# Performance work log

Measured on AMD Instinct MI355X. Metric: run time of the kernel, lower is better.

Reference implementation:

```python
import jax, jax.numpy as jnp
import numpy as np

DIM = 3072
HEADS = 24
HEAD_DIM = 128
MLP_HIDDEN = int(DIM * 3.0)   # 9216
EPS = 1e-6
B, S = 1, 4096


def setup_inputs() -> dict:
    key = jax.random.key(0)
    ks = jax.random.split(key, 9)
    fused_out = 3 * DIM + 2 * MLP_HIDDEN  # 27648
    std_in = 1.0 / np.sqrt(DIM)
    return {
        "hidden_states": jax.random.normal(ks[0], (B, S, DIM), jnp.float32),
        "temb_mod": jax.random.normal(ks[1], (B, 3 * DIM), jnp.float32),
        "rotary_cos": jax.random.uniform(ks[2], (S, HEAD_DIM), jnp.float32),
        "rotary_sin": jax.random.uniform(ks[3], (S, HEAD_DIM), jnp.float32),
        "w_qkv_mlp": jax.random.normal(ks[4], (DIM, fused_out), jnp.float32) * std_in,
        "w_out_attn": jax.random.normal(ks[5], (DIM, DIM), jnp.float32) * std_in,
        "w_out_mlp": jax.random.normal(ks[6], (MLP_HIDDEN, DIM), jnp.float32) * (1.0 / np.sqrt(MLP_HIDDEN)),
        "norm_q_w": jnp.ones((HEAD_DIM,), jnp.float32),
        "norm_k_w": jnp.ones((HEAD_DIM,), jnp.float32),
    }


def _rms_norm(x, w):
    var = jnp.mean(jnp.square(x), axis=-1, keepdims=True)
    return x * jax.lax.rsqrt(var + EPS) * w


def _apply_rope(x, cos, sin):
    # x: [B,H,S,D]; cos/sin: [S,D]. Interleaved (diffusers FLUX) rotation.
    xr = x.reshape(*x.shape[:-1], HEAD_DIM // 2, 2)
    x_re, x_im = xr[..., 0], xr[..., 1]
    x_rot = jnp.stack([-x_im, x_re], axis=-1).reshape(x.shape)
    return x * cos + x_rot * sin


def reference(hidden_states, temb_mod, rotary_cos, rotary_sin,
              w_qkv_mlp, w_out_attn, w_out_mlp, norm_q_w, norm_k_w):
    residual = hidden_states
    # modulation split: shift, scale, gate each [B,1,D]
    shift, scale, gate = jnp.split(temb_mod[:, None, :], 3, axis=-1)
    # LayerNorm (no affine)
    mu = jnp.mean(hidden_states, axis=-1, keepdims=True)
    var = jnp.mean(jnp.square(hidden_states - mu), axis=-1, keepdims=True)
    ln = (hidden_states - mu) * jax.lax.rsqrt(var + EPS)
    h = ln * (1.0 + scale) + shift
    # fused QKV + MLP projection
    qkv_mlp = jnp.einsum('bsd,df->bsf', h, w_qkv_mlp)
    qkv, mlp_gate_up = jnp.split(qkv_mlp, [3 * DIM], axis=-1)
    q, k, v = jnp.split(qkv, 3, axis=-1)
    to_heads = lambda t: t.reshape(B, S, HEADS, HEAD_DIM).transpose(0, 2, 1, 3)
    q, k, v = to_heads(q), to_heads(k), to_heads(v)
    q = _apply_rope(_rms_norm(q, norm_q_w), rotary_cos, rotary_sin)
    k = _apply_rope(_rms_norm(k, norm_k_w), rotary_cos, rotary_sin)
    # attention
    scores = jnp.einsum('bhqd,bhkd->bhqk', q, k) / np.sqrt(HEAD_DIM).astype(np.float32)
    attn = jnp.einsum('bhqk,bhkd->bhqd', jax.nn.softmax(scores, axis=-1), v)
    attn = attn.transpose(0, 2, 1, 3).reshape(B, S, DIM)
    # SwiGLU
    a, b = jnp.split(mlp_gate_up, 2, axis=-1)
    mlp_out = jax.nn.silu(a) * b
    out = jnp.einsum('bsd,de->bse', attn, w_out_attn) + jnp.einsum('bsm,md->bsd', mlp_out, w_out_mlp)
    return residual + gate * out
```

## Files before the change

kernel.cpp:

```cpp
#include <hip/hip_runtime.h>
#include <stdint.h>
#include <math.h>

#define DIM 3072
#define SEQ 4096
#define NH 24
#define HD 128
#define MLP 9216
#define FUSED 27648
#define SD FUSED
#define K2 12288

typedef __attribute__((ext_vector_type(8))) short short8;
typedef __attribute__((ext_vector_type(4))) float f32x4;

__device__ __forceinline__ float bf2f(uint16_t b){ uint32_t x = ((uint32_t)b)<<16; return __builtin_bit_cast(float,x); }
__device__ __forceinline__ uint16_t f2bf(float f){
  uint32_t x = __builtin_bit_cast(uint32_t,f);
  x += 0x7fffu + ((x>>16)&1u);
  return (uint16_t)(x>>16);
}
__device__ __forceinline__ void gl_lds16(const void* g, void* l){
  __builtin_amdgcn_global_load_lds((const __attribute__((address_space(1))) void*)g,
                                   (__attribute__((address_space(3))) void*)l, 16, 0, 0);
}

__global__ __launch_bounds__(256) void castT_kernel(const float* __restrict__ src,
                                                    uint16_t* __restrict__ dst,
                                                    int K, int N, int dstStride){
  __shared__ float tile[32][33];
  int t = threadIdx.x;
  int n0 = blockIdx.x<<5, k0 = blockIdx.y<<5;
  int r = t>>3, c4 = (t&7)<<2;
  float4 v = *(const float4*)&src[(size_t)(k0+r)*N + n0 + c4];
  tile[r][c4] = v.x; tile[r][c4+1] = v.y; tile[r][c4+2] = v.z; tile[r][c4+3] = v.w;
  __syncthreads();
  int n = t>>3, kc = (t&7)<<2;
  ushort4 o;
  o.x = f2bf(tile[kc  ][n]);
  o.y = f2bf(tile[kc+1][n]);
  o.z = f2bf(tile[kc+2][n]);
  o.w = f2bf(tile[kc+3][n]);
  *(ushort4*)&dst[(size_t)(n0+n)*dstStride + k0 + kc] = o;
}

__global__ __launch_bounds__(256) void ln_mod_kernel(const float* __restrict__ x,
                                                     const float* __restrict__ temb,
                                                     uint16_t* __restrict__ h){
  int s = blockIdx.x;
  int t = threadIdx.x;
  const float4* row = (const float4*)(x + (size_t)s*DIM);
  float4 v[3];
  float sum=0.f, ss=0.f;
  #pragma unroll
  for (int i=0;i<3;i++){
    v[i] = row[t + i*256];
    sum += v[i].x+v[i].y+v[i].z+v[i].w;
    ss  += v[i].x*v[i].x + v[i].y*v[i].y + v[i].z*v[i].z + v[i].w*v[i].w;
  }
  #pragma unroll
  for (int off=32; off; off>>=1){ sum += __shfl_xor(sum, off, 64); ss += __shfl_xor(ss, off, 64); }
  __shared__ float red[8];
  int lane = t&63, w = t>>6;
  if (lane==0){ red[w]=sum; red[w+4]=ss; }
  __syncthreads();
  sum = red[0]+red[1]+red[2]+red[3];
  ss  = red[4]+red[5]+red[6]+red[7];
  float mu = sum*(1.f/DIM);
  float var = ss*(1.f/DIM) - mu*mu;
  float rs = rsqrtf(var + 1e-6f);
  uint16_t* hrow = h + (size_t)s*DIM;
  #pragma unroll
  for (int i=0;i<3;i++){
    int c = (t + i*256)*4;
    float4 sc = *(const float4*)&temb[DIM + c];
    float4 sh = *(const float4*)&temb[c];
    ushort4 o;
    o.x = f2bf((v[i].x - mu)*rs*(1.f+sc.x) + sh.x);
    o.y = f2bf((v[i].y - mu)*rs*(1.f+sc.y) + sh.y);
    o.z = f2bf((v[i].z - mu)*rs*(1.f+sc.z) + sh.z);
    o.w = f2bf((v[i].w - mu)*rs*(1.f+sc.w) + sh.w);
    *(ushort4*)&hrow[c] = o;
  }
}

#define STAGE_HT(SRC, LDSB, KOFF) do{ \
    gl_lds16((SRC) + (KOFF), (LDSB) + (size_t)t*8); \
    gl_lds16((SRC) + r64K + (KOFF), (LDSB) + (size_t)(t+512)*8); \
  }while(0)

#define GPHASE(MI0, MI1, STG, WAITV) do{ \
    short8 a00 = *(const short8*)&Ab[(MI0)*1024 + pk0]; \
    short8 a01 = *(const short8*)&Ab[(MI0)*1024 + pk1]; \
    short8 a10 = *(const short8*)&Ab[(MI1)*1024 + pk0]; \
    short8 a11 = *(const short8*)&Ab[(MI1)*1024 + pk1]; \
    STG; \
    __builtin_amdgcn_s_barrier(); \
    asm volatile("s_waitcnt lgkmcnt(0)" ::: "memory"); \
    __builtin_amdgcn_s_setprio(1); \
    _Pragma("unroll") \
    for (int ni=0; ni<4; ni++){ \
      acc[MI0][ni] = __builtin_amdgcn_mfma_f32_16x16x32_bf16(a00, bfr[ni][0], acc[MI0][ni], 0,0,0); \
      acc[MI1][ni] = __builtin_amdgcn_mfma_f32_16x16x32_bf16(a10, bfr[ni][0], acc[MI1][ni], 0,0,0); \
      acc[MI0][ni] = __builtin_amdgcn_mfma_f32_16x16x32_bf16(a01, bfr[ni][1], acc[MI0][ni], 0,0,0); \
      acc[MI1][ni] = __builtin_amdgcn_mfma_f32_16x16x32_bf16(a11, bfr[ni][1], acc[MI1][ni], 0,0,0); \
    } \
    __builtin_amdgcn_s_setprio(0); \
    WAITV \
    __builtin_amdgcn_s_barrier(); \
  }while(0)

template<bool OUT_BF16, bool FINAL>
__global__ __launch_bounds__(512,2) void gemm256_kernel(const uint16_t* __restrict__ A,
                                                        const uint16_t* __restrict__ BT,
                                                        void* __restrict__ Cout,
                                                        const float* __restrict__ resid,
                                                        const float* __restrict__ temb,
                                                        int M, int N, int K){
  __shared__ alignas(16) uint16_t As[2][2][128*64];
  __shared__ alignas(16) uint16_t Bs[2][2][128*64];
  const int t = threadIdx.x, lane = t&63, w = t>>6;
  const int G = gridDim.x, cpx = G>>3;
  const int b = blockIdx.x;
  const int b2 = (b&7)*cpx + (b>>3);
  const int mt = M>>8;
  const int n_t = b2/mt, m_t = b2 - n_t*mt;
  const size_t m0 = (size_t)m_t<<8, n0 = (size_t)n_t<<8;
  const int wm = (w>>2)<<7, wn = (w&3)<<6;
  const int lr = lane&15, q4 = lane>>4;
  const int r0 = t>>3;
  const int g0 = (t&7) ^ (r0&7);
  const uint16_t* Asrc = A  + (m0 + r0)*(size_t)K + g0*8;
  const uint16_t* Bsrc = BT + (n0 + r0)*(size_t)K + g0*8;
  const size_t r64K = (size_t)64*K, r128K = (size_t)128*K;
  const int halfA = w>>2, halfB = (w&3)>>1, rbB = wn&64;
  const uint16_t* ArdBase = &As[0][halfA][0] + lr*64;
  const uint16_t* BrdBase = &Bs[0][halfB][0] + (rbB+lr)*64;
  const int x7 = lr&7;
  const int pk0 = (q4^x7)<<3, pk1 = ((q4|4)^x7)<<3;
  STAGE_HT(Bsrc, &Bs[0][0][0], (size_t)0);
  STAGE_HT(Bsrc, &Bs[0][1][0], r128K);
  STAGE_HT(Asrc, &As[0][0][0], (size_t)0);
  STAGE_HT(Asrc, &As[0][1][0], r128K);
  STAGE_HT(Bsrc, &Bs[1][0][0], (size_t)64);
  STAGE_HT(Bsrc, &Bs[1][1][0], r128K + 64);
  asm volatile("s_waitcnt vmcnt(4)" ::: "memory");
  __builtin_amdgcn_s_barrier();
  f32x4 acc[8][4] = {};
  const int NT = K>>6;
  for (int T=0; T<NT; ++T){
    const int cur = T&1, nxt = cur^1;
    const uint16_t* Ab = ArdBase + (cur<<14);
    const uint16_t* Bb = BrdBase + (cur<<14);
    uint16_t* AsN0 = &As[nxt][0][0]; uint16_t* AsN1 = &As[nxt][1][0];
    uint16_t* BsC0 = &Bs[cur][0][0]; uint16_t* BsC1 = &Bs[cur][1][0];
    const bool stA = (T+1<NT), stB = (T+2<NT);
    const size_t kA = (size_t)(T+1)<<6, kB = (size_t)(T+2)<<6;
    short8 bfr[4][2];
    #pragma unroll
    for (int ni=0; ni<4; ni++){
      bfr[ni][0] = *(const short8*)&Bb[ni*1024 + pk0];
      bfr[ni][1] = *(const short8*)&Bb[ni*1024 + pk1];
    }
    GPHASE(0,1, if(stA){ STAGE_HT(Asrc, AsN0, kA); }, ;);
    GPHASE(2,3, if(stA){ STAGE_HT(Asrc, AsN1, kA + r128K); }, ;);
    GPHASE(4,5, if(stB){ STAGE_HT(Bsrc, BsC0, kB); }, ;);
    GPHASE(6,7, if(stB){ STAGE_HT(Bsrc, BsC1, kB + r128K); },
           if(stB){ asm volatile("s_waitcnt vmcnt(4)" ::: "memory"); }
           else   { asm volatile("s_waitcnt vmcnt(0)" ::: "memory"); });
  }
  #pragma unroll
  for (int mi=0; mi<8; mi++){
    #pragma unroll
    for (int ni=0; ni<4; ni++){
      const size_t col = n0 + wn + ni*16 + lr;
      const float gate = FINAL ? temb[2*DIM + col] : 0.f;
      #pragma unroll
      for (int r=0; r<4; r++){
        const size_t row = m0 + wm + mi*16 + (q4<<2) + r;
        const size_t idx = row*(size_t)N + col;
        float vv = acc[mi][ni][r];
        if (FINAL) vv = resid[idx] + gate*vv;
        if (OUT_BF16) ((uint16_t*)Cout)[idx] = f2bf(vv);
        else          ((float*)Cout)[idx] = vv;
      }
    }
  }
}

__global__ __launch_bounds__(256) void qk_rope_kernel(uint16_t* __restrict__ qkv,
                                                      const float* __restrict__ cosb,
                                                      const float* __restrict__ sinb,
                                                      const float* __restrict__ wq,
                                                      const float* __restrict__ wk){
  int t = threadIdx.x, lane = t&63, w = t>>6;
  int pair = blockIdx.x*4 + w;
  int s = pair/24, hh = pair - s*24;
  int d0 = lane*2;
  float c0 = cosb[s*HD + d0], c1 = cosb[s*HD + d0+1];
  float sn0 = sinb[s*HD + d0], sn1 = sinb[s*HD + d0+1];
  #pragma unroll
  for (int which=0; which<2; ++which){
    uint16_t* p = qkv + (size_t)s*SD + which*DIM + hh*HD + d0;
    const float* ww = which ? wk : wq;
    uint32_t u = *(const uint32_t*)p;
    float x0 = bf2f((uint16_t)(u&0xffffu)), x1 = bf2f((uint16_t)(u>>16));
    float ssum = x0*x0 + x1*x1;
    #pragma unroll
    for (int off=32; off; off>>=1) ssum += __shfl_xor(ssum, off, 64);
    float r = rsqrtf(ssum*(1.f/HD) + 1e-6f);
    float xn0 = x0*r*ww[d0], xn1 = x1*r*ww[d0+1];
    float y0 = xn0*c0 - xn1*sn0;
    float y1 = xn1*c1 + xn0*sn1;
    *(uint32_t*)p = (uint32_t)f2bf(y0) | ((uint32_t)f2bf(y1)<<16);
  }
}

__global__ __launch_bounds__(256) void attn_kernel(const uint16_t* __restrict__ qkv,
                                                   uint16_t* __restrict__ out){
  __shared__ alignas(16) uint16_t QP[64*128];
  __shared__ alignas(16) uint16_t Ks[64*128];
  __shared__ alignas(16) uint16_t Vt[128*64];
  int t = threadIdx.x, lane = t&63, w = t>>6;
  int q0 = blockIdx.x<<6, h = blockIdx.y;
  int lr = lane&15, q4 = lane>>4, lk = q4<<3;
  const uint16_t* qb = qkv + (size_t)q0*SD + h*HD;
  #pragma unroll
  for (int i=0;i<4;i++){
    int c = t + i*256;
    gl_lds16((const char*)(qb + (size_t)(c>>4)*SD) + ((c&15)<<4), (char*)QP + c*16);
  }
  __syncthreads();
  short8 qf[4];
  #pragma unroll
  for (int kc=0;kc<4;kc++) qf[kc] = *(const short8*)&QP[(w*16+lr)*128 + kc*32 + lk];
  __syncthreads();
  float m_q = -3.0e38f, l_q = 0.f;
  f32x4 o[8] = {};
  const uint16_t* kb = qkv + (size_t)DIM + h*HD;
  const uint16_t* vb = qkv + (size_t)(2*DIM) + h*HD;
  uint16_t* Pw = QP + w*(16*64);
  const float scale = 0.08838834764831845f;
  for (int kt=0; kt<64; ++kt){
    const uint16_t* kbt = kb + (size_t)(kt<<6)*SD;
    const uint16_t* vbt = vb + (size_t)(kt<<6)*SD;
    __syncthreads();
    #pragma unroll
    for (int i=0;i<4;i++){
      int c = t + i*256;
      int row = c>>4, gd = c&15;
      gl_lds16((const char*)(kbt + (size_t)row*SD) + (((gd ^ (row&15))&15)<<4),
               (char*)Ks + c*16);
    }
    #pragma unroll
    for (int i=0;i<8;i++){
      int idx = t + i*256;
      int rp = idx>>6;
      int k0 = rp<<1, d0 = lane<<1;
      uint32_t u0 = *(const uint32_t*)(vbt + (size_t)k0*SD + d0);
      uint32_t u1 = *(const uint32_t*)(vbt + (size_t)(k0+1)*SD + d0);
      int pos = (((rp>>2) ^ (lane&7))<<3) + (k0&7);
      *(uint32_t*)&Vt[(d0<<6) + pos]     = (u0&0xffffu) | (u1<<16);
      *(uint32_t*)&Vt[((d0+1)<<6) + pos] = (u0>>16) | (u1&0xffff0000u);
    }
    __syncthreads();
    f32x4 ta[4];
    __builtin_amdgcn_s_setprio(1);
    #pragma unroll
    for (int nk=0;nk<4;nk++){
      ta[nk] = (f32x4){0.f,0.f,0.f,0.f};
      #pragma unroll
      for (int kc=0;kc<4;kc++){
        short8 kf = *(const short8*)&Ks[(nk*16+lr)*128 + (((kc*4+q4) ^ lr)<<3)];
        ta[nk] = __builtin_amdgcn_mfma_f32_16x16x32_bf16(kf, qf[kc], ta[nk], 0,0,0);
      }
      ta[nk] *= scale;
    }
    __builtin_amdgcn_s_setprio(0);
    float mx01 = fmaxf(fmaxf(ta[0][0],ta[0][1]), fmaxf(ta[0][2],ta[0][3]));
    float mx23 = fmaxf(fmaxf(ta[1][0],ta[1][1]), fmaxf(ta[1][2],ta[1][3]));
    float mx45 = fmaxf(fmaxf(ta[2][0],ta[2][1]), fmaxf(ta[2][2],ta[2][3]));
    float mx67 = fmaxf(fmaxf(ta[3][0],ta[3][1]), fmaxf(ta[3][2],ta[3][3]));
    float pmax = fmaxf(fmaxf(mx01,mx23), fmaxf(mx45,mx67));
    pmax = fmaxf(pmax, __shfl_xor(pmax, 16, 64));
    pmax = fmaxf(pmax, __shfl_xor(pmax, 32, 64));
    int skip = __all(pmax <= m_q + 8.f);
    float alpha_q = 1.f;
    if (!skip){
      float mnew = fmaxf(m_q, pmax);
      alpha_q = __expf(m_q - mnew);
      m_q = mnew;
    }
    float psum = 0.f;
    #pragma unroll
    for (int nk=0;nk<4;nk++){
      float p0 = __expf(ta[nk][0] - m_q);
      float p1 = __expf(ta[nk][1] - m_q);
      float p2 = __expf(ta[nk][2] - m_q);
      float p3 = __expf(ta[nk][3] - m_q);
      psum += (p0+p1)+(p2+p3);
      uint32_t lo = (uint32_t)f2bf(p0) | ((uint32_t)f2bf(p1)<<16);
      uint32_t hi = (uint32_t)f2bf(p2) | ((uint32_t)f2bf(p3)<<16);
      int k0 = nk*16 + (q4<<2);
      uint2 pk; pk.x = lo; pk.y = hi;
      *(uint2*)&Pw[lr*64 + ((((k0>>3) ^ lr)&7)<<3) + (k0&7)] = pk;
    }
    psum += __shfl_xor(psum, 16, 64);
    psum += __shfl_xor(psum, 32, 64);
    l_q = l_q*alpha_q + psum;
    if (!skip){
      float aR0 = __shfl(alpha_q, (q4<<2)+0, 64);
      float aR1 = __shfl(alpha_q, (q4<<2)+1, 64);
      float aR2 = __shfl(alpha_q, (q4<<2)+2, 64);
      float aR3 = __shfl(alpha_q, (q4<<2)+3, 64);
      #pragma unroll
      for (int nd=0;nd<8;nd++){
        f32x4 t4 = o[nd];
        t4[0]*=aR0; t4[1]*=aR1; t4[2]*=aR2; t4[3]*=aR3;
        o[nd]=t4;
      }
    }
    __builtin_amdgcn_s_setprio(1);
    #pragma unroll
    for (int kc=0;kc<2;kc++){
      short8 pf = *(const short8*)&Pw[lr*64 + ((((kc*4+q4) ^ lr)&7)<<3)];
      #pragma unroll
      for (int nd=0;nd<8;nd++){
        int d = nd*16 + lr;
        short8 vf = *(const short8*)&Vt[(d<<6) + ((((kc*4+q4) ^ ((lr>>1)&7)))<<3)];
        o[nd] = __builtin_amdgcn_mfma_f32_16x16x32_bf16(pf, vf, o[nd], 0,0,0);
      }
    }
    __builtin_amdgcn_s_setprio(0);
  }
  float linv0 = 1.f/__shfl(l_q, (q4<<2)+0, 64);
  float linv1 = 1.f/__shfl(l_q, (q4<<2)+1, 64);
  float linv2 = 1.f/__shfl(l_q, (q4<<2)+2, 64);
  float linv3 = 1.f/__shfl(l_q, (q4<<2)+3, 64);
  uint16_t* ob = out + (size_t)(q0 + w*16)*K2 + h*HD;
  #pragma unroll
  for (int nd=0;nd<8;nd++){
    ob[(size_t)(q4*4 + 0)*K2 + nd*16 + lr] = f2bf(o[nd][0]*linv0);
    ob[(size_t)(q4*4 + 1)*K2 + nd*16 + lr] = f2bf(o[nd][1]*linv1);
    ob[(size_t)(q4*4 + 2)*K2 + nd*16 + lr] = f2bf(o[nd][2]*linv2);
    ob[(size_t)(q4*4 + 3)*K2 + nd*16 + lr] = f2bf(o[nd][3]*linv3);
  }
}

__global__ __launch_bounds__(256) void swiglu_kernel(const uint16_t* __restrict__ qkv,
                                                     uint16_t* __restrict__ mlp){
  size_t idx = ((size_t)blockIdx.x*256 + threadIdx.x)*4;
  size_t s = idx/MLP, j = idx - s*MLP;
  const uint16_t* pa = qkv + s*SD + 3*DIM + j;
  const uint16_t* pb = pa + MLP;
  ushort4 ua = *(const ushort4*)pa, ub = *(const ushort4*)pb;
  ushort4 o;
  float a, b;
  a = bf2f(ua.x); b = bf2f(ub.x); o.x = f2bf(a*b/(1.f+__expf(-a)));
  a = bf2f(ua.y); b = bf2f(ub.y); o.y = f2bf(a*b/(1.f+__expf(-a)));
  a = bf2f(ua.z); b = bf2f(ub.z); o.z = f2bf(a*b/(1.f+__expf(-a)));
  a = bf2f(ua.w); b = bf2f(ub.w); o.w = f2bf(a*b/(1.f+__expf(-a)));
  *(ushort4*)(mlp + s*K2 + j) = o;
}

extern "C" void kernel_launch(void* const* d_in, const int* in_sizes, int n_in,
                              void* d_out, int out_size, void* d_ws, size_t ws_size,
                              hipStream_t stream){
  (void)in_sizes; (void)n_in; (void)out_size;
  const float* hs   = (const float*)d_in[0];
  const float* temb = (const float*)d_in[1];
  const float* rcos = (const float*)d_in[2];
  const float* rsin = (const float*)d_in[3];
  const float* w1   = (const float*)d_in[4];
  const float* wa   = (const float*)d_in[5];
  const float* wm   = (const float*)d_in[6];
  const float* nqw  = (const float*)d_in[7];
  const float* nkw  = (const float*)d_in[8];

  char* ws = (char*)d_ws;
  const size_t off_w1T  = 0;
  const size_t off_woT  = 169869312ULL;
  const size_t off_h    = 245366784ULL;
  const size_t off_qkv  = 270532608ULL;
  const size_t off_ap   = 497025024ULL;
  const size_t needed   = 597688320ULL;
  if (ws_size < needed) return;

  uint16_t* w1T  = (uint16_t*)(ws + off_w1T);
  uint16_t* woT  = (uint16_t*)(ws + off_woT);
  uint16_t* hbuf = (uint16_t*)(ws + off_h);
  uint16_t* qkv  = (uint16_t*)(ws + off_qkv);
  uint16_t* ap   = (uint16_t*)(ws + off_ap);

  castT_kernel<<<dim3(FUSED/32, DIM/32), 256, 0, stream>>>(w1, w1T, DIM, FUSED, DIM);
  castT_kernel<<<dim3(DIM/32,  DIM/32),  256, 0, stream>>>(wa, woT, DIM, DIM, K2);
  castT_kernel<<<dim3(DIM/32,  MLP/32),  256, 0, stream>>>(wm, woT + DIM, MLP, DIM, K2);
  ln_mod_kernel<<<SEQ, 256, 0, stream>>>(hs, temb, hbuf);
  gemm256_kernel<true,false><<<(SEQ/256)*(FUSED/256), 512, 0, stream>>>(hbuf, w1T, qkv, nullptr, nullptr, SEQ, FUSED, DIM);
  qk_rope_kernel<<<SEQ*NH/4, 256, 0, stream>>>(qkv, rcos, rsin, nqw, nkw);
  attn_kernel<<<dim3(SEQ/64, NH), 256, 0, stream>>>(qkv, ap);
  swiglu_kernel<<<(SEQ*(size_t)MLP/4)/256, 256, 0, stream>>>(qkv, ap + DIM);
  gemm256_kernel<false,true><<<(SEQ/256)*(DIM/256), 512, 0, stream>>>(ap, woT, d_out, hs, temb, SEQ, DIM, K2);
}
```

Measured before the change: 2.289 ms.

## Double-buffer K/V tiles in attention to overlap loads with MFMA compute

The attention kernel now keeps two LDS buffers each for K and transposed V. It issues the next tile's K global-to-LDS loads and V register loads before computing on the current tile, then writes the transposed V into the alternate buffer after the PV MFMAs. This hides global memory latency behind compute and drops one barrier per iteration. In exchange it doubles LDS use, from 48KB to 80KB per block, which may cut occupancy, and adds register pressure for the staged V values.

```diff
diff --git a/kernel.cpp b/kernel.cpp
--- a/kernel.cpp
+++ b/kernel.cpp
@@ -219,51 +219,72 @@
 __global__ __launch_bounds__(256) void attn_kernel(const uint16_t* __restrict__ qkv,
                                                    uint16_t* __restrict__ out){
   __shared__ alignas(16) uint16_t QP[64*128];
-  __shared__ alignas(16) uint16_t Ks[64*128];
-  __shared__ alignas(16) uint16_t Vt[128*64];
+  __shared__ alignas(16) uint16_t Ks[2][64*128];
+  __shared__ alignas(16) uint16_t Vt[2][128*64];
   int t = threadIdx.x, lane = t&63, w = t>>6;
   int q0 = blockIdx.x<<6, h = blockIdx.y;
   int lr = lane&15, q4 = lane>>4, lk = q4<<3;
   const uint16_t* qb = qkv + (size_t)q0*SD + h*HD;
+  const uint16_t* kb = qkv + (size_t)DIM + h*HD;
+  const uint16_t* vb = qkv + (size_t)(2*DIM) + h*HD;
   #pragma unroll
   for (int i=0;i<4;i++){
     int c = t + i*256;
     gl_lds16((const char*)(qb + (size_t)(c>>4)*SD) + ((c&15)<<4), (char*)QP + c*16);
   }
+  #pragma unroll
+  for (int i=0;i<4;i++){
+    int c = t + i*256;
+    int row = c>>4, gd = c&15;
+    gl_lds16((const char*)(kb + (size_t)row*SD) + (((gd ^ (row&15))&15)<<4),
+             (char*)Ks[0] + c*16);
+  }
+  uint32_t vr0[8], vr1[8];
+  #pragma unroll
+  for (int i=0;i<8;i++){
+    int rp = w + i*4;
+    int k0 = rp<<1, d0 = lane<<1;
+    vr0[i] = *(const uint32_t*)(vb + (size_t)k0*SD + d0);
+    vr1[i] = *(const uint32_t*)(vb + (size_t)(k0+1)*SD + d0);
+  }
   __syncthreads();
   short8 qf[4];
   #pragma unroll
   for (int kc=0;kc<4;kc++) qf[kc] = *(const short8*)&QP[(w*16+lr)*128 + kc*32 + lk];
+  #pragma unroll
+  for (int i=0;i<8;i++){
+    int rp = w + i*4;
+    int k0 = rp<<1, d0 = lane<<1;
+    int pos = (((rp>>2) ^ (lane&7))<<3) + (k0&7);
+    *(uint32_t*)&Vt[0][(d0<<6) + pos]     = (vr0[i]&0xffffu) | (vr1[i]<<16);
+    *(uint32_t*)&Vt[0][((d0+1)<<6) + pos] = (vr0[i]>>16) | (vr1[i]&0xffff0000u);
+  }
   __syncthreads();
   float m_q = -3.0e38f, l_q = 0.f;
   f32x4 o[8] = {};
-  const uint16_t* kb = qkv + (size_t)DIM + h*HD;
-  const uint16_t* vb = qkv + (size_t)(2*DIM) + h*HD;
   uint16_t* Pw = QP + w*(16*64);
   const float scale = 0.08838834764831845f;
   for (int kt=0; kt<64; ++kt){
-    const uint16_t* kbt = kb + (size_t)(kt<<6)*SD;
-    const uint16_t* vbt = vb + (size_t)(kt<<6)*SD;
-    __syncthreads();
-    #pragma unroll
-    for (int i=0;i<4;i++){
-      int c = t + i*256;
-      int row = c>>4, gd = c&15;
-      gl_lds16((const char*)(kbt + (size_t)row*SD) + (((gd ^ (row&15))&15)<<4),
-               (char*)Ks + c*16);
-    }
-    #pragma unroll
-    for (int i=0;i<8;i++){
-      int idx = t + i*256;
-      int rp = idx>>6;
-      int k0 = rp<<1, d0 = lane<<1;
-      uint32_t u0 = *(const uint32_t*)(vbt + (size_t)k0*SD + d0);
-      uint32_t u1 = *(const uint32_t*)(vbt + (size_t)(k0+1)*SD + d0);
-      int pos = (((rp>>2) ^ (lane&7))<<3) + (k0&7);
-      *(uint32_t*)&Vt[(d0<<6) + pos]     = (u0&0xffffu) | (u1<<16);
-      *(uint32_t*)&Vt[((d0+1)<<6) + pos] = (u0>>16) | (u1&0xffff0000u);
-    }
-    __syncthreads();
+    const int cur = kt&1, nxt = cur^1;
+    const bool more = (kt+1 < 64);
+    if (more){
+      const uint16_t* kbt = kb + (size_t)((kt+1)<<6)*SD;
+      const uint16_t* vbt = vb + (size_t)((kt+1)<<6)*SD;
+      #pragma unroll
+      for (int i=0;i<4;i++){
+        int c = t + i*256;
+        int row = c>>4, gd = c&15;
+        gl_lds16((const char*)(kbt + (size_t)row*SD) + (((gd ^ (row&15))&15)<<4),
+                 (char*)Ks[nxt] + c*16);
+      }
+      #pragma unroll
+      for (int i=0;i<8;i++){
+        int rp = w + i*4;
+        int k0 = rp<<1, d0 = lane<<1;
+        vr0[i] = *(const uint32_t*)(vbt + (size_t)k0*SD + d0);
+        vr1[i] = *(const uint32_t*)(vbt + (size_t)(k0+1)*SD + d0);
+      }
+    }
     f32x4 ta[4];
     __builtin_amdgcn_s_setprio(1);
     #pragma unroll
@@ -271,7 +292,7 @@
       ta[nk] = (f32x4){0.f,0.f,0.f,0.f};
       #pragma unroll
       for (int kc=0;kc<4;kc++){
-        short8 kf = *(const short8*)&Ks[(nk*16+lr)*128 + (((kc*4+q4) ^ lr)<<3)];
+        short8 kf = *(const short8*)&Ks[cur][(nk*16+lr)*128 + (((kc*4+q4) ^ lr)<<3)];
         ta[nk] = __builtin_amdgcn_mfma_f32_16x16x32_bf16(kf, qf[kc], ta[nk], 0,0,0);
       }
       ta[nk] *= scale;
@@ -327,11 +348,23 @@
       #pragma unroll
       for (int nd=0;nd<8;nd++){
         int d = nd*16 + lr;
-        short8 vf = *(const short8*)&Vt[(d<<6) + ((((kc*4+q4) ^ ((lr>>1)&7)))<<3)];
+        short8 vf = *(const short8*)&Vt[cur][(d<<6) + ((((kc*4+q4) ^ ((lr>>1)&7)))<<3)];
         o[nd] = __builtin_amdgcn_mfma_f32_16x16x32_bf16(pf, vf, o[nd], 0,0,0);
       }
     }
     __builtin_amdgcn_s_setprio(0);
+    if (more){
+      asm volatile("s_waitcnt vmcnt(0)" ::: "memory");
+      #pragma unroll
+      for (int i=0;i<8;i++){
+        int rp = w + i*4;
+        int k0 = rp<<1, d0 = lane<<1;
+        int pos = (((rp>>2) ^ (lane&7))<<3) + (k0&7);
+        *(uint32_t*)&Vt[nxt][(d0<<6) + pos]     = (vr0[i]&0xffffu) | (vr1[i]<<16);
+        *(uint32_t*)&Vt[nxt][((d0+1)<<6) + pos] = (vr0[i]>>16) | (vr1[i]&0xffff0000u);
+      }
+    }
+    __syncthreads();
   }
   float linv0 = 1.f/__shfl(l_q, (q4<<2)+0, 64);
   float linv1 = 1.f/__shfl(l_q, (q4<<2)+1, 64);
```

New measurement: 2.273 ms. About the same (-0.7%).
